# Performance work log

Measured on AMD Instinct MI355X. Metric: run time of the kernel, lower is better.

## Reference

```python
import jax, jax.numpy as jnp
import numpy as np

B, S, E = 2, 2048, 1024
H, D = 16, 64
BASE = 10000.0


def rotate_half(x):
    x1, x2 = jnp.split(x, 2, axis=-1)
    return jnp.concatenate((-x2, x1), axis=-1)


def rope_cos_sin(seq_len, dim):
    inv_freq = 1.0 / (BASE ** (jnp.arange(0, dim, 2, dtype=jnp.float32) / dim))
    t = jnp.arange(seq_len, dtype=jnp.float32)
    freqs = jnp.einsum('i,j->ij', t, inv_freq)          # [S, D/2]
    emb = jnp.concatenate((freqs, freqs), axis=-1)       # [S, D]
    return jnp.cos(emb), jnp.sin(emb)


def setup_inputs() -> dict:
    key = jax.random.key(0)
    ks = jax.random.split(key, 9)
    s = 1.0 / np.sqrt(E)
    inp = {
        'x': jax.random.normal(ks[0], (B, S, E), dtype=jnp.float32),
        'mask': jnp.ones((B, S), dtype=jnp.int32),
        'Wq': jax.random.normal(ks[1], (E, H * D), dtype=jnp.float32) * s,
        'bq': jnp.zeros((H * D,), dtype=jnp.float32),
        'Wk': jax.random.normal(ks[2], (E, H * D), dtype=jnp.float32) * s,
        'bk': jnp.zeros((H * D,), dtype=jnp.float32),
        'Wv': jax.random.normal(ks[3], (E, H * D), dtype=jnp.float32) * s,
        'bv': jnp.zeros((H * D,), dtype=jnp.float32),
        'Wo': jax.random.normal(ks[4], (H * D, E), dtype=jnp.float32) * s,
        'bo': jnp.zeros((E,), dtype=jnp.float32),
    }
    return inp


def reference(x, mask, Wq, bq, Wk, bk, Wv, bv, Wo, bo):
    b, s, _ = x.shape
    scale = D ** (-0.5)
    # projections -> [B, H, S, D]
    q = (x @ Wq + bq).reshape(b, s, H, D).transpose(0, 2, 1, 3)
    k = (x @ Wk + bk).reshape(b, s, H, D).transpose(0, 2, 1, 3)
    v = (x @ Wv + bv).reshape(b, s, H, D).transpose(0, 2, 1, 3)
    # rotary position embedding
    cos, sin = rope_cos_sin(s, D)                      # [S, D]
    cos = cos[None, None]
    sin = sin[None, None]
    q = q * cos + rotate_half(q) * sin
    k = k * cos + rotate_half(k) * sin
    # scores [B, H, S, S]
    scores = jnp.einsum('bhqd,bhkd->bhqk', q, k) * scale
    # padding mask [B,1,1,S]
    scores = jnp.where(mask[:, None, None, :] == 0, -jnp.inf, scores)
    # causal mask
    i = jnp.arange(s)
    causal = jnp.where(i[None, :] > i[:, None], -jnp.inf, 0.0)  # [S, S]
    scores = scores + causal[None, None]
    attn = jax.nn.softmax(scores, axis=-1)
    ctx = jnp.einsum('bhqk,bhkd->bhqd', attn, v)
    ctx = ctx.transpose(0, 2, 1, 3).reshape(b, s, H * D)
    return ctx @ Wo + bo
```

## Files before the change

### kernel.cpp

```cpp
#include <hip/hip_runtime.h>
#include <cstdint>
#include <cstddef>

#define DEVI __device__ __forceinline__

typedef __bf16 bf16_t;
typedef __bf16 bf16x4 __attribute__((ext_vector_type(4)));
typedef __bf16 bf16x8 __attribute__((ext_vector_type(8)));
typedef float  f32x4  __attribute__((ext_vector_type(4)));
typedef unsigned short u16x4 __attribute__((ext_vector_type(4)));

static constexpr int Bz = 2, S = 2048, E = 1024, H = 16, Dh = 64;
static constexpr int M  = Bz * S;
static constexpr int N  = H * Dh;
static constexpr int Kd = E;

DEVI unsigned short f2bf(float f) {
  unsigned u = __builtin_bit_cast(unsigned, f);
  return (unsigned short)((u + 0x7fffu + ((u >> 16) & 1u)) >> 16);
}

DEVI void async_copy16(void* lds, const void* g) {
  __builtin_amdgcn_global_load_lds((__attribute__((address_space(1))) void*)(g),
                                   (__attribute__((address_space(3))) void*)(lds), 16, 0, 0);
}

__global__ void prep_kernel(const float* __restrict__ x, bf16_t* __restrict__ xb,
                            const float* __restrict__ Wq, const float* __restrict__ Wk,
                            const float* __restrict__ Wv, const float* __restrict__ Wo,
                            bf16_t* __restrict__ WtBase,
                            float* __restrict__ ropeC, float* __restrict__ ropeS) {
  __shared__ unsigned short tile[64][68];
  const int blk = blockIdx.x, tid = threadIdx.x;
  if (blk < 4096) {
    int i = blk * 256 + tid;
    float4 v = ((const float4*)x)[i];
    u16x4 o = { f2bf(v.x), f2bf(v.y), f2bf(v.z), f2bf(v.w) };
    ((u16x4*)xb)[i] = o;
  } else if (blk < 5120) {
    const int i = blk - 4096;
    const int z = i >> 8, rest = i & 255;
    const int n0 = (rest & 15) * 64, k0 = (rest >> 4) * 64;
    const float* W = (z == 0) ? Wq : (z == 1) ? Wk : (z == 2) ? Wv : Wo;
    unsigned short* T = (unsigned short*)(WtBase + (size_t)z * Kd * N);
    for (int e = tid; e < 1024; e += 256) {
      int r = e >> 4, c4 = (e & 15) * 4;
      float4 v = *(const float4*)(W + (size_t)(k0 + r) * N + n0 + c4);
      u16x4 o = { f2bf(v.x), f2bf(v.y), f2bf(v.z), f2bf(v.w) };
      *(u16x4*)&tile[r][c4] = o;
    }
    __syncthreads();
    for (int e = tid; e < 1024; e += 256) {
      int r = e >> 4, c4 = (e & 15) * 4;
      u16x4 o = { tile[c4][r], tile[c4 + 1][r], tile[c4 + 2][r], tile[c4 + 3][r] };
      *(u16x4*)&T[(size_t)(n0 + r) * Kd + k0 + c4] = o;
    }
  } else {
    int i = (blk - 5120) * 256 + tid;
    int pos = i >> 5, j = i & 31;
    float inv = exp2f(-(float)j * 0.41524101186092029f);
    float ang = (float)pos * inv;
    ropeC[i] = cosf(ang);
    ropeS[i] = sinf(ang);
  }
}


DEVI void gemm_mainloop(const bf16_t* __restrict__ A, const bf16_t* __restrict__ Bt,
                        bf16_t* sA, bf16_t* sB, int m0, int n0, f32x4 (&acc)[4][4]) {
  const int tid  = threadIdx.x;
  const int lane = tid & 63;
  const int wid  = tid >> 6;
  const int l16  = lane & 15;
  const int quad = lane >> 4;
  const int wm = (wid >> 1) * 64;
  const int wn = (wid & 1) * 64;
  const int o0 = wid * 2048 + lane * 16;
  const int o1 = o0 + 1024;
  const int r0 = o0 >> 6, c0 = o0 & 63;
  const int r1 = o1 >> 6, c1 = o1 & 63;
  const char* Ab = (const char*)A;
  const char* Bb = (const char*)Bt;
  char* sAc = (char*)sA;
  char* sBc = (char*)sB;

  for (int k0 = 0; k0 < Kd; k0 += 32) {
    __syncthreads();
    async_copy16(sAc + wid * 2048,        Ab + ((size_t)(m0 + r0) * Kd + k0) * 2 + c0);
    async_copy16(sAc + wid * 2048 + 1024, Ab + ((size_t)(m0 + r1) * Kd + k0) * 2 + c1);
    async_copy16(sBc + wid * 2048,        Bb + ((size_t)(n0 + r0) * Kd + k0) * 2 + c0);
    async_copy16(sBc + wid * 2048 + 1024, Bb + ((size_t)(n0 + r1) * Kd + k0) * 2 + c1);
    __syncthreads();
    bf16x8 af[4], bfv[4];
#pragma unroll
    for (int mi = 0; mi < 4; ++mi)
      af[mi] = *(const bf16x8*)(sA + (wm + mi * 16 + l16) * 32 + quad * 8);
#pragma unroll
    for (int ni = 0; ni < 4; ++ni)
      bfv[ni] = *(const bf16x8*)(sB + (wn + ni * 16 + l16) * 32 + quad * 8);
#pragma unroll
    for (int mi = 0; mi < 4; ++mi)
#pragma unroll
      for (int ni = 0; ni < 4; ++ni)
        acc[mi][ni] = __builtin_amdgcn_mfma_f32_16x16x32_bf16(af[mi], bfv[ni], acc[mi][ni], 0, 0, 0);
  }
}

__global__ __launch_bounds__(256, 3) void gemm_qkv_kernel(
    const bf16_t* __restrict__ xb, const bf16_t* __restrict__ WtBase,
    const float* __restrict__ bq, const float* __restrict__ bk, const float* __restrict__ bv,
    bf16_t* __restrict__ outBase, bf16_t* __restrict__ Vt,
    const float* __restrict__ ropeC, const float* __restrict__ ropeS) {
  __shared__ bf16_t sM[8192];
  const int z = blockIdx.z;
  const bf16_t* Bt = WtBase + (size_t)z * Kd * N;
  const float* bias = (z == 0) ? bq : (z == 1) ? bk : bv;
  const int n0 = blockIdx.x * 128, m0 = blockIdx.y * 128;
  f32x4 acc[4][4] = {};
  gemm_mainloop(xb, Bt, sM, sM + 4096, m0, n0, acc);

  const int tid = threadIdx.x, lane = tid & 63, wid = tid >> 6;
  const int l16 = lane & 15, quad = lane >> 4;
  const int wm = (wid >> 1) * 64, wn = (wid & 1) * 64;
  const int cbase = n0 + wn;
  const int h = cbase >> 6;

  if (z < 2) {
    unsigned short* outp = (unsigned short*)(outBase + (size_t)z * M * N);
    const float qs = (z == 0) ? 0.18033688011112042f : 1.0f;
#pragma unroll
    for (int mi = 0; mi < 4; ++mi)
#pragma unroll
      for (int r = 0; r < 4; ++r) {
        int t = m0 + wm + mi * 16 + quad * 4 + r;
        int bb = t >> 11, s = t & (S - 1);
        size_t obase = ((size_t)(bb * H + h) * S + s) * Dh;
#pragma unroll
        for (int np = 0; np < 2; ++np) {
          int j = np * 16 + l16;
          float cc = ropeC[s * 32 + j];
          float ss = ropeS[s * 32 + j];
          float xlo = acc[mi][np][r]     + bias[cbase + j];
          float xhi = acc[mi][np + 2][r] + bias[cbase + j + 32];
          outp[obase + j]      = f2bf((xlo * cc - xhi * ss) * qs);
          outp[obase + j + 32] = f2bf((xhi * cc + xlo * ss) * qs);
        }
      }
  } else {
    const int bb = m0 >> 11, s0 = m0 & (S - 1);
    const int head0 = n0 >> 6;
    const int myh = wid & 1;
    for (int hh = 0; hh < 2; ++hh)
      for (int dq = 0; dq < 2; ++dq) {
        __syncthreads();
        if (myh == hh) {
#pragma unroll
          for (int ni2 = 0; ni2 < 2; ++ni2) {
            int ni = dq * 2 + ni2;
            int dloc = ni2 * 16 + l16;
            float bv_ = bias[cbase + ni * 16 + l16];
#pragma unroll
            for (int mi = 0; mi < 4; ++mi)
#pragma unroll
              for (int r = 0; r < 4; ++r) {
                int tloc = wm + mi * 16 + quad * 4 + r;
                sM[dloc * 136 + tloc] = (bf16_t)(acc[mi][ni][r] + bv_);
              }
          }
        }
        __syncthreads();
#pragma unroll
        for (int rep = 0; rep < 2; ++rep) {
          int cidx = rep * 256 + tid;
          int dloc = cidx >> 4, chunk = cidx & 15;
          bf16x8 v = *(const bf16x8*)&sM[dloc * 136 + chunk * 8];
          size_t off = ((size_t)(bb * H + head0 + hh) * Dh + dq * 32 + dloc) * S + s0 + chunk * 8;
          *(bf16x8*)(Vt + off) = v;
        }
      }
  }
}

__global__ __launch_bounds__(256, 4) void gemm_o_kernel(
    const bf16_t* __restrict__ A, const bf16_t* __restrict__ Bt,
    const float* __restrict__ bias, float* __restrict__ out) {
  __shared__ bf16_t sA[2048], sB[4096];
  const int n0 = blockIdx.x * 128, m0 = blockIdx.y * 64;
  const int tid = threadIdx.x, lane = tid & 63, wid = tid >> 6;
  const int l16 = lane & 15, quad = lane >> 4;
  const int wm = (wid >> 1) * 32, wn = (wid & 1) * 64;
  const int rowoff = lane >> 2, col8 = (lane & 3) * 8;
  const char* Ab = (const char*)A;
  const char* Bb = (const char*)Bt;
  char* sAc = (char*)sA;
  char* sBc = (char*)sB;
  f32x4 acc[2][4] = {};

  for (int k0 = 0; k0 < Kd; k0 += 32) {
    __syncthreads();
    async_copy16(sAc + wid * 1024,
                 Ab + ((size_t)(m0 + wid * 16 + rowoff) * Kd + k0 + col8) * 2);
    async_copy16(sBc + (wid * 2) * 1024,
                 Bb + ((size_t)(n0 + wid * 32 + rowoff) * Kd + k0 + col8) * 2);
    async_copy16(sBc + (wid * 2 + 1) * 1024,
                 Bb + ((size_t)(n0 + wid * 32 + 16 + rowoff) * Kd + k0 + col8) * 2);
    __syncthreads();
    bf16x8 af[2], bfv[4];
#pragma unroll
    for (int mi = 0; mi < 2; ++mi)
      af[mi] = *(const bf16x8*)(sA + (wm + mi * 16 + l16) * 32 + quad * 8);
#pragma unroll
    for (int ni = 0; ni < 4; ++ni)
      bfv[ni] = *(const bf16x8*)(sB + (wn + ni * 16 + l16) * 32 + quad * 8);
#pragma unroll
    for (int mi = 0; mi < 2; ++mi)
#pragma unroll
      for (int ni = 0; ni < 4; ++ni)
        acc[mi][ni] = __builtin_amdgcn_mfma_f32_16x16x32_bf16(af[mi], bfv[ni], acc[mi][ni], 0, 0, 0);
  }
#pragma unroll
  for (int mi = 0; mi < 2; ++mi)
#pragma unroll
    for (int r = 0; r < 4; ++r) {
      int t = m0 + wm + mi * 16 + quad * 4 + r;
#pragma unroll
      for (int ni = 0; ni < 4; ++ni) {
        int c = n0 + wn + ni * 16 + l16;
        out[(size_t)t * N + c] = acc[mi][ni][r] + bias[c];
      }
    }
}

__global__ __launch_bounds__(256, 3) void attn_kernel(
    const bf16_t* __restrict__ Q, const bf16_t* __restrict__ Kb,
    const bf16_t* __restrict__ Vt, const int* __restrict__ mask,
    bf16_t* __restrict__ ctx) {
  __shared__ bf16_t sK[2][4096];
  __shared__ bf16_t sV[2][4096];
  __shared__ unsigned short sP[4][16 * 72];

  const int tid = threadIdx.x, lane = tid & 63, wid = tid >> 6;
  const int l16 = lane & 15, quad = lane >> 4;

  const int idx = blockIdx.x;
  const int qb  = 31 - (idx >> 5);
  const int bh  = idx & 31;
  const int b   = bh >> 4;
  const int q0  = qb * 64;
  const int qw  = q0 + wid * 16;

  const bf16_t* Qp = Q + ((size_t)bh * S + qw) * Dh;
  const char*   Kg = (const char*)(Kb + (size_t)bh * S * Dh);
  const char*   Vg = (const char*)(Vt + (size_t)bh * Dh * S);
  const int*    mp = mask + b * S;

  bf16x8 qf0 = *(const bf16x8*)(Qp + l16 * Dh + quad * 8);
  bf16x8 qf1 = *(const bf16x8*)(Qp + l16 * Dh + 32 + quad * 8);

  const size_t kOff0 = ((size_t)(wid * 16 + l16) * Dh + quad * 8) * 2;
  const size_t kOff1 = kOff0 + 64;
  const size_t vOff0 = ((size_t)(wid * 16 + l16) * S + quad * 8) * 2;
  const size_t vOff1 = vOff0 + 64;
  char* sKc = (char*)sK;
  char* sVc = (char*)sV;

  auto stage = [&](int buf, int kt) {
    size_t kbK = (size_t)kt * 64 * Dh * 2;
    size_t kbV = (size_t)kt * 64 * 2;
    async_copy16(sKc + buf * 8192 + wid * 2048,        Kg + kbK + kOff0);
    async_copy16(sKc + buf * 8192 + wid * 2048 + 1024, Kg + kbK + kOff1);
    async_copy16(sVc + buf * 8192 + wid * 2048,        Vg + kbV + vOff0);
    async_copy16(sVc + buf * 8192 + wid * 2048 + 1024, Vg + kbV + vOff1);
  };

  f32x4 acc[4] = {};
  float lsum = 0.f;
  const int qcol = qw + l16;
  const int niter = qb + 1;
  unsigned short* pb = &sP[wid][0];

  stage(0, 0);
  for (int kt = 0; kt < niter; ++kt) {
    const int kb = kt * 64;
    __syncthreads();
    int mk = mp[kb + lane];
    if (kt + 1 < niter) stage((kt + 1) & 1, kt + 1);
    const bf16_t* kbuf = &sK[kt & 1][0];
    const bf16_t* vbuf = &sV[kt & 1][0];

    f32x4 st[4];
#pragma unroll
    for (int g = 0; g < 4; ++g) {
      bf16x8 kf0 = *(const bf16x8*)(kbuf + (g * 2 + 0) * 512 + lane * 8);
      bf16x8 kf1 = *(const bf16x8*)(kbuf + (g * 2 + 1) * 512 + lane * 8);
      f32x4 z = {};
      z = __builtin_amdgcn_mfma_f32_16x16x32_bf16(kf0, qf0, z, 0, 0, 0);
      z = __builtin_amdgcn_mfma_f32_16x16x32_bf16(kf1, qf1, z, 0, 0, 0);
      st[g] = z;
    }

    unsigned long long dm = __ballot(mk == 0);
    if (dm) {
#pragma unroll
      for (int g = 0; g < 4; ++g)
#pragma unroll
        for (int r = 0; r < 4; ++r)
          if ((dm >> (g * 16 + quad * 4 + r)) & 1ull) st[g][r] = -1e30f;
    }
    if (kt == niter - 1) {
#pragma unroll
      for (int g = 0; g < 4; ++g)
#pragma unroll
        for (int r = 0; r < 4; ++r)
          if (kb + g * 16 + quad * 4 + r > qcol) st[g][r] = -1e30f;
    }

#pragma unroll
    for (int g = 0; g < 4; ++g) {
      float e0 = exp2f(st[g][0]), e1 = exp2f(st[g][1]);
      float e2 = exp2f(st[g][2]), e3 = exp2f(st[g][3]);
      lsum += (e0 + e1) + (e2 + e3);
      bf16x4 pk = { (bf16_t)e0, (bf16_t)e1, (bf16_t)e2, (bf16_t)e3 };
      *(bf16x4*)&pb[l16 * 72 + g * 16 + quad * 4] = pk;
    }
    bf16x8 pf0 = *(const bf16x8*)((const bf16_t*)(const void*)pb + l16 * 72 + quad * 8);
    bf16x8 pf1 = *(const bf16x8*)((const bf16_t*)(const void*)pb + l16 * 72 + 32 + quad * 8);

#pragma unroll
    for (int dt = 0; dt < 4; ++dt) {
      bf16x8 vf0 = *(const bf16x8*)(vbuf + (dt * 2 + 0) * 512 + lane * 8);
      bf16x8 vf1 = *(const bf16x8*)(vbuf + (dt * 2 + 1) * 512 + lane * 8);
      acc[dt] = __builtin_amdgcn_mfma_f32_16x16x32_bf16(vf0, pf0, acc[dt], 0, 0, 0);
      acc[dt] = __builtin_amdgcn_mfma_f32_16x16x32_bf16(vf1, pf1, acc[dt], 0, 0, 0);
    }
  }

  lsum += __shfl_xor(lsum, 16);
  lsum += __shfl_xor(lsum, 32);
  float inv = 1.0f / lsum;
  unsigned short* cp = (unsigned short*)ctx;
  size_t trow = ((size_t)(b * S + qw + l16)) * N + (size_t)(bh & 15) * Dh;
#pragma unroll
  for (int dt = 0; dt < 4; ++dt) {
    u16x4 o = { f2bf(acc[dt][0] * inv), f2bf(acc[dt][1] * inv),
                f2bf(acc[dt][2] * inv), f2bf(acc[dt][3] * inv) };
    *(u16x4*)&cp[trow + dt * 16 + quad * 4] = o;
  }
}


extern "C" void kernel_launch(void* const* d_in, const int* in_sizes, int n_in,
                              void* d_out, int out_size, void* d_ws, size_t ws_size,
                              hipStream_t stream) {
  const float* x  = (const float*)d_in[0];
  const int*  msk = (const int*)d_in[1];
  const float* Wq = (const float*)d_in[2];
  const float* bq = (const float*)d_in[3];
  const float* Wk = (const float*)d_in[4];
  const float* bk = (const float*)d_in[5];
  const float* Wv = (const float*)d_in[6];
  const float* bv = (const float*)d_in[7];
  const float* Wo = (const float*)d_in[8];
  const float* bo = (const float*)d_in[9];
  float* out = (float*)d_out;
  (void)in_sizes; (void)n_in; (void)out_size; (void)ws_size;

  char* ws = (char*)d_ws;
  bf16_t* xb   = (bf16_t*)(ws);
  bf16_t* WT   = (bf16_t*)(ws + (8u  << 20));
  bf16_t* Qb   = (bf16_t*)(ws + (16u << 20));
  bf16_t* Kbuf = (bf16_t*)(ws + (24u << 20));
  bf16_t* Vt   = (bf16_t*)(ws + (32u << 20));
  float* ropeC = (float*)(ws + (40u << 20));
  float* ropeS = ropeC + (size_t)S * 32;
  bf16_t* ctx  = (bf16_t*)(ws + (41u << 20));

  prep_kernel<<<5376, 256, 0, stream>>>(x, xb, Wq, Wk, Wv, Wo, WT, ropeC, ropeS);
  gemm_qkv_kernel<<<dim3(8, 32, 3), 256, 0, stream>>>(xb, WT, bq, bk, bv, Qb, Vt, ropeC, ropeS);
  attn_kernel<<<1024, 256, 0, stream>>>(Qb, Kbuf, Vt, msk, ctx);
  gemm_o_kernel<<<dim3(8, 64), 256, 0, stream>>>(ctx, WT + (size_t)3 * Kd * N, bo, out);
}
```

Baseline: 204.9 us.

## Restructure attention: 2 waves with 32 query rows each, P kept in registers

The attention kernel now runs 128-thread blocks where each wave handles 32 query rows (two 16-row sub-tiles), so each K/V fragment read from LDS is reused twice. The softmax probabilities stay in registers and feed 16x16x16 MFMAs directly instead of round-tripping through an LDS scratch buffer. The K/V double buffer is replaced by a single buffer with two barriers per iteration, which removes the copy/compute overlap. The aim is to cut LDS traffic and shared memory use, at the cost of exposed load latency, a smaller instruction shape for the PV product, and fewer waves per block.

```diff
diff --git a/kernel.cpp b/kernel.cpp
--- a/kernel.cpp
+++ b/kernel.cpp
@@ -7,6 +7,7 @@
 typedef __bf16 bf16_t;
 typedef __bf16 bf16x4 __attribute__((ext_vector_type(4)));
 typedef __bf16 bf16x8 __attribute__((ext_vector_type(8)));
+typedef short  s16x4  __attribute__((ext_vector_type(4)));
 typedef float  f32x4  __attribute__((ext_vector_type(4)));
 typedef unsigned short u16x4 __attribute__((ext_vector_type(4)));
 
@@ -23,6 +24,18 @@
 DEVI void async_copy16(void* lds, const void* g) {
   __builtin_amdgcn_global_load_lds((__attribute__((address_space(1))) void*)(g),
                                    (__attribute__((address_space(3))) void*)(lds), 16, 0, 0);
+}
+
+DEVI f32x4 mfma16(bf16x4 a, bf16x4 b, f32x4 c) {
+#if __has_builtin(__builtin_amdgcn_mfma_f32_16x16x16bf16_1k)
+  return __builtin_amdgcn_mfma_f32_16x16x16bf16_1k(
+      __builtin_bit_cast(s16x4, a), __builtin_bit_cast(s16x4, b), c, 0, 0, 0);
+#elif __has_builtin(__builtin_amdgcn_mfma_f32_16x16x16_bf16)
+  return __builtin_amdgcn_mfma_f32_16x16x16_bf16(a, b, c, 0, 0, 0);
+#else
+  asm("v_mfma_f32_16x16x16_bf16 %0, %1, %2, %0" : "+v"(c) : "v"(a), "v"(b));
+  return c;
+#endif
 }
 
 __global__ void prep_kernel(const float* __restrict__ x, bf16_t* __restrict__ xb,
@@ -231,13 +244,11 @@
     }
 }
 
-__global__ __launch_bounds__(256, 3) void attn_kernel(
+__global__ __launch_bounds__(128, 4) void attn_kernel(
     const bf16_t* __restrict__ Q, const bf16_t* __restrict__ Kb,
     const bf16_t* __restrict__ Vt, const int* __restrict__ mask,
     bf16_t* __restrict__ ctx) {
-  __shared__ bf16_t sK[2][4096];
-  __shared__ bf16_t sV[2][4096];
-  __shared__ unsigned short sP[4][16 * 72];
+  __shared__ bf16_t sKV[8192];
 
   const int tid = threadIdx.x, lane = tid & 63, wid = tid >> 6;
   const int l16 = lane & 15, quad = lane >> 4;
@@ -247,104 +258,105 @@
   const int bh  = idx & 31;
   const int b   = bh >> 4;
   const int q0  = qb * 64;
-  const int qw  = q0 + wid * 16;
+  const int qw  = q0 + wid * 32;
 
   const bf16_t* Qp = Q + ((size_t)bh * S + qw) * Dh;
   const char*   Kg = (const char*)(Kb + (size_t)bh * S * Dh);
   const char*   Vg = (const char*)(Vt + (size_t)bh * Dh * S);
   const int*    mp = mask + b * S;
 
-  bf16x8 qf0 = *(const bf16x8*)(Qp + l16 * Dh + quad * 8);
-  bf16x8 qf1 = *(const bf16x8*)(Qp + l16 * Dh + 32 + quad * 8);
-
-  const size_t kOff0 = ((size_t)(wid * 16 + l16) * Dh + quad * 8) * 2;
-  const size_t kOff1 = kOff0 + 64;
-  const size_t vOff0 = ((size_t)(wid * 16 + l16) * S + quad * 8) * 2;
-  const size_t vOff1 = vOff0 + 64;
-  char* sKc = (char*)sK;
-  char* sVc = (char*)sV;
-
-  auto stage = [&](int buf, int kt) {
-    size_t kbK = (size_t)kt * 64 * Dh * 2;
-    size_t kbV = (size_t)kt * 64 * 2;
-    async_copy16(sKc + buf * 8192 + wid * 2048,        Kg + kbK + kOff0);
-    async_copy16(sKc + buf * 8192 + wid * 2048 + 1024, Kg + kbK + kOff1);
-    async_copy16(sVc + buf * 8192 + wid * 2048,        Vg + kbV + vOff0);
-    async_copy16(sVc + buf * 8192 + wid * 2048 + 1024, Vg + kbV + vOff1);
-  };
-
-  f32x4 acc[4] = {};
-  float lsum = 0.f;
-  const int qcol = qw + l16;
+  bf16x8 qf[2][2];
+#pragma unroll
+  for (int qs = 0; qs < 2; ++qs)
+#pragma unroll
+    for (int ch = 0; ch < 2; ++ch)
+      qf[qs][ch] = *(const bf16x8*)(Qp + (qs * 16 + l16) * Dh + ch * 32 + quad * 8);
+
+  size_t kSrc[4], vSrc[4];
+  int dstK[4], dstV[4];
+#pragma unroll
+  for (int i = 0; i < 4; ++i) {
+    int sk = wid * 4 + i;
+    kSrc[i] = ((size_t)((sk >> 1) * 16 + l16) * Dh + (sk & 1) * 32 + quad * 8) * 2;
+    dstK[i] = sk * 1024;
+    vSrc[i] = ((size_t)((sk >> 1) * 16 + l16) * S + (sk & 1) * 32 + quad * 8) * 2;
+    dstV[i] = 8192 + sk * 1024;
+  }
+  char* sc = (char*)sKV;
+
+  f32x4 acc[2][4] = {};
+  float lsum[2] = { 0.f, 0.f };
   const int niter = qb + 1;
-  unsigned short* pb = &sP[wid][0];
-
-  stage(0, 0);
+
   for (int kt = 0; kt < niter; ++kt) {
     const int kb = kt * 64;
     __syncthreads();
+#pragma unroll
+    for (int i = 0; i < 4; ++i) {
+      async_copy16(sc + dstK[i], Kg + (size_t)kb * 128 + kSrc[i]);
+      async_copy16(sc + dstV[i], Vg + (size_t)kb * 2 + vSrc[i]);
+    }
     int mk = mp[kb + lane];
-    if (kt + 1 < niter) stage((kt + 1) & 1, kt + 1);
-    const bf16_t* kbuf = &sK[kt & 1][0];
-    const bf16_t* vbuf = &sV[kt & 1][0];
-
-    f32x4 st[4];
+    __syncthreads();
+
+    unsigned long long dm = __ballot(mk == 0);
+    const bool last = (kt == niter - 1);
+
+    bf16x4 pf[2][4];
 #pragma unroll
     for (int g = 0; g < 4; ++g) {
-      bf16x8 kf0 = *(const bf16x8*)(kbuf + (g * 2 + 0) * 512 + lane * 8);
-      bf16x8 kf1 = *(const bf16x8*)(kbuf + (g * 2 + 1) * 512 + lane * 8);
-      f32x4 z = {};
-      z = __builtin_amdgcn_mfma_f32_16x16x32_bf16(kf0, qf0, z, 0, 0, 0);
-      z = __builtin_amdgcn_mfma_f32_16x16x32_bf16(kf1, qf1, z, 0, 0, 0);
-      st[g] = z;
-    }
-
-    unsigned long long dm = __ballot(mk == 0);
-    if (dm) {
-#pragma unroll
-      for (int g = 0; g < 4; ++g)
-#pragma unroll
-        for (int r = 0; r < 4; ++r)
-          if ((dm >> (g * 16 + quad * 4 + r)) & 1ull) st[g][r] = -1e30f;
-    }
-    if (kt == niter - 1) {
-#pragma unroll
-      for (int g = 0; g < 4; ++g)
-#pragma unroll
-        for (int r = 0; r < 4; ++r)
-          if (kb + g * 16 + quad * 4 + r > qcol) st[g][r] = -1e30f;
-    }
-
-#pragma unroll
-    for (int g = 0; g < 4; ++g) {
-      float e0 = exp2f(st[g][0]), e1 = exp2f(st[g][1]);
-      float e2 = exp2f(st[g][2]), e3 = exp2f(st[g][3]);
-      lsum += (e0 + e1) + (e2 + e3);
-      bf16x4 pk = { (bf16_t)e0, (bf16_t)e1, (bf16_t)e2, (bf16_t)e3 };
-      *(bf16x4*)&pb[l16 * 72 + g * 16 + quad * 4] = pk;
-    }
-    bf16x8 pf0 = *(const bf16x8*)((const bf16_t*)(const void*)pb + l16 * 72 + quad * 8);
-    bf16x8 pf1 = *(const bf16x8*)((const bf16_t*)(const void*)pb + l16 * 72 + 32 + quad * 8);
-
+      bf16x8 kf0 = *(const bf16x8*)(sKV + (g * 2 + 0) * 512 + lane * 8);
+      bf16x8 kf1 = *(const bf16x8*)(sKV + (g * 2 + 1) * 512 + lane * 8);
+#pragma unroll
+      for (int qs = 0; qs < 2; ++qs) {
+        f32x4 z = {};
+        z = __builtin_amdgcn_mfma_f32_16x16x32_bf16(kf0, qf[qs][0], z, 0, 0, 0);
+        z = __builtin_amdgcn_mfma_f32_16x16x32_bf16(kf1, qf[qs][1], z, 0, 0, 0);
+        if (dm) {
+#pragma unroll
+          for (int r = 0; r < 4; ++r)
+            if ((dm >> (g * 16 + quad * 4 + r)) & 1ull) z[r] = -1e30f;
+        }
+        if (last) {
+          int qcol = qw + qs * 16 + l16;
+#pragma unroll
+          for (int r = 0; r < 4; ++r)
+            if (kb + g * 16 + quad * 4 + r > qcol) z[r] = -1e30f;
+        }
+        float e0 = exp2f(z[0]), e1 = exp2f(z[1]);
+        float e2 = exp2f(z[2]), e3 = exp2f(z[3]);
+        lsum[qs] += (e0 + e1) + (e2 + e3);
+        pf[qs][g] = (bf16x4){ (bf16_t)e0, (bf16_t)e1, (bf16_t)e2, (bf16_t)e3 };
+      }
+    }
+
+#pragma unroll
+    for (int dt = 0; dt < 4; ++dt)
+#pragma unroll
+      for (int g = 0; g < 4; ++g) {
+        bf16x4 vf = *(const bf16x4*)(sKV + 4096 + (dt * 2 + (g >> 1)) * 512 +
+                                     (((g & 1) * 2 + (quad >> 1)) * 16 + l16) * 8 +
+                                     (quad & 1) * 4);
+        acc[0][dt] = mfma16(vf, pf[0][g], acc[0][dt]);
+        acc[1][dt] = mfma16(vf, pf[1][g], acc[1][dt]);
+      }
+  }
+
+  asm volatile("s_nop 7\ns_nop 7" :::);
+  unsigned short* cp = (unsigned short*)ctx;
+#pragma unroll
+  for (int qs = 0; qs < 2; ++qs) {
+    float ls = lsum[qs];
+    ls += __shfl_xor(ls, 16);
+    ls += __shfl_xor(ls, 32);
+    float inv = 1.0f / ls;
+    size_t trow = ((size_t)(b * S + qw + qs * 16 + l16)) * N + (size_t)(bh & 15) * Dh;
 #pragma unroll
     for (int dt = 0; dt < 4; ++dt) {
-      bf16x8 vf0 = *(const bf16x8*)(vbuf + (dt * 2 + 0) * 512 + lane * 8);
-      bf16x8 vf1 = *(const bf16x8*)(vbuf + (dt * 2 + 1) * 512 + lane * 8);
-      acc[dt] = __builtin_amdgcn_mfma_f32_16x16x32_bf16(vf0, pf0, acc[dt], 0, 0, 0);
-      acc[dt] = __builtin_amdgcn_mfma_f32_16x16x32_bf16(vf1, pf1, acc[dt], 0, 0, 0);
-    }
-  }
-
-  lsum += __shfl_xor(lsum, 16);
-  lsum += __shfl_xor(lsum, 32);
-  float inv = 1.0f / lsum;
-  unsigned short* cp = (unsigned short*)ctx;
-  size_t trow = ((size_t)(b * S + qw + l16)) * N + (size_t)(bh & 15) * Dh;
-#pragma unroll
-  for (int dt = 0; dt < 4; ++dt) {
-    u16x4 o = { f2bf(acc[dt][0] * inv), f2bf(acc[dt][1] * inv),
-                f2bf(acc[dt][2] * inv), f2bf(acc[dt][3] * inv) };
-    *(u16x4*)&cp[trow + dt * 16 + quad * 4] = o;
+      u16x4 o = { f2bf(acc[qs][dt][0] * inv), f2bf(acc[qs][dt][1] * inv),
+                  f2bf(acc[qs][dt][2] * inv), f2bf(acc[qs][dt][3] * inv) };
+      *(u16x4*)&cp[trow + dt * 16 + quad * 4] = o;
+    }
   }
 }
 
@@ -377,6 +389,6 @@
 
   prep_kernel<<<5376, 256, 0, stream>>>(x, xb, Wq, Wk, Wv, Wo, WT, ropeC, ropeS);
   gemm_qkv_kernel<<<dim3(8, 32, 3), 256, 0, stream>>>(xb, WT, bq, bk, bv, Qb, Vt, ropeC, ropeS);
-  attn_kernel<<<1024, 256, 0, stream>>>(Qb, Kbuf, Vt, msk, ctx);
+  attn_kernel<<<1024, 128, 0, stream>>>(Qb, Kbuf, Vt, msk, ctx);
   gemm_o_kernel<<<dim3(8, 64), 256, 0, stream>>>(ctx, WT + (size_t)3 * Kd * N, bo, out);
 }
```

After: 246.7 us. 1.2x slower.
